# Performance work log

Measured on AMD Instinct MI355X. Metric: run time of the kernel, lower is better.

## Reference

```python
import jax, jax.numpy as jnp
import numpy as np

K = 3
STRIDE = 1
PADDING = 1
INVALID = -1.0


def _unfold(x, k, stride, padding, fill):
    # x: [B, C, H, W] -> patches [B, C, k, k, P] matching torch F.unfold ordering
    x = jnp.pad(x, ((0, 0), (0, 0), (padding, padding), (padding, padding)),
                constant_values=fill)
    # feature dim ordered channel-major (C, kh, kw), same as torch unfold
    p = jax.lax.conv_general_dilated_patches(x, (k, k), (stride, stride), 'VALID')
    b, _, ho, wo = p.shape
    c = x.shape[1]
    return p.reshape(b, c, k, k, ho * wo), ho, wo


def setup_inputs() -> dict:
    key = jax.random.key(0)
    k1, k2, k3, k4 = jax.random.split(key, 4)
    B, C, H, W = 8, 64, 128, 128
    OC = 64
    inp = jax.random.normal(k1, (B, C, H, W), dtype=jnp.float32)
    mask = jax.random.randint(k2, (B, H, W), 0, 4).astype(jnp.float32)
    conv = jax.random.normal(k3, (OC, C, K, K), dtype=jnp.float32) * 0.05
    bias = jax.random.normal(k4, (OC,), dtype=jnp.float32) * 0.05
    return {"inp": inp, "mask": mask, "conv": conv, "bias": bias}


def reference(inp, mask, conv, bias):
    k, stride, padding = K, STRIDE, PADDING
    b, c, h_in, w_in = inp.shape
    oc = conv.shape[0]
    center = (k - 1) // 2

    inp_patched, ho, wo = _unfold(inp, k, stride, padding, INVALID)       # [B,C,k,k,P]
    mask_patched, _, _ = _unfold(mask[:, None], k, stride, padding, INVALID)  # [B,1,k,k,P]
    mask_patched = mask_patched[:, 0]                                      # [B,k,k,P]

    center_val = mask_patched[:, center:center + 1, center:center + 1, :]  # [B,1,1,P]
    mask_eq = (mask_patched == center_val).astype(inp.dtype)               # [B,k,k,P]

    masked_input = inp_patched * mask_eq[:, None]                          # [B,C,k,k,P]
    m_norm = (k * k) / jnp.clip(mask_eq.reshape(b, k * k, -1).sum(axis=1), 1e-8)  # [B,P]

    masked_input = masked_input.reshape(b, c, k * k, -1)                   # [B,C,kk,P]
    w = conv.reshape(oc, c, k * k)                                         # [O,C,kk]
    out = jnp.einsum('bcxp,ocx->bop', masked_input, w)                     # [B,O,P]
    out = out * m_norm[:, None, :]
    out = out.reshape(b, oc, ho, wo)
    out = out + bias[None, :, None, None]

    mask_out = mask_patched[:, center, center, :].reshape(b, 1, ho, wo)
    return out, mask_out
```

## Files before the change

kernel.cpp:

```cpp
#include <hip/hip_runtime.h>
#include <stdint.h>

#define HW   128
#define CIN  64
#define OCN  64
#define NB   8

typedef __attribute__((ext_vector_type(8)))  short short8;
typedef __attribute__((ext_vector_type(16))) float floatx16;
typedef unsigned long long u64;

union F8 { short8 s; u64 u[2]; uint32_t d[4]; uint4 q; };

static __device__ __forceinline__ ushort f2bf(float f) {
    uint32_t u = __float_as_uint(f);
    uint32_t r = (u + 0x7FFFu + ((u >> 16) & 1u)) >> 16;
    return (ushort)r;
}

__global__ void wprep_kernel(const float* __restrict__ conv, ushort* __restrict__ wb) {
    int idx = blockIdx.x * 256 + threadIdx.x;
    int tap = idx >> 12;
    int r   = idx & 4095;
    int oc  = r >> 6;
    int c   = r & 63;
    wb[idx] = f2bf(conv[(oc * 64 + c) * 9 + tap]);
}

#define XS_CSTR 68
#define XS_ROW  (HW * XS_CSTR)
#define LDS_BYTES 72192

__global__ __launch_bounds__(256, 2)
void iconv_main(const float* __restrict__ inp, const float* __restrict__ mask,
                const ushort* __restrict__ wb, const float* __restrict__ bias,
                float* __restrict__ out)
{
    extern __shared__ char smem[];
    ushort* Xs = (ushort*)smem;
    float*  Ms = (float*)(smem + 69632);
    float*  Bb = (float*)(smem + 69632 + 2048);

    const int tid  = threadIdx.x;
    const int bb   = blockIdx.x >> 6;
    const int y0   = (blockIdx.x & 63) << 1;
    const int lane = tid & 63;
    const int l31  = lane & 31;
    const int lh   = lane >> 5;
    const int w    = tid >> 6;
    const int yloc = w >> 1;
    const int xw   = (w & 1) * 64;
    const int y    = y0 + yloc;

    {
        const int cp = tid & 31;
        const int xq = (tid >> 5) * 16;
        const float* base0 = inp + ((size_t)(bb * CIN + 2 * cp) * HW) * HW;
        #pragma unroll
        for (int rr = 0; rr < 4; ++rr) {
            int gy = y0 - 1 + rr;
            if (gy >= 0 && gy < HW) {
                const float4* q0 = (const float4*)(base0 + (size_t)gy * HW + xq);
                const float4* q1 = (const float4*)(base0 + (size_t)HW * HW + (size_t)gy * HW + xq);
                float4 v0[4], v1[4];
                #pragma unroll
                for (int i = 0; i < 4; ++i) { v0[i] = q0[i]; v1[i] = q1[i]; }
                ushort* xrow = Xs + rr * XS_ROW + xq * XS_CSTR + 2 * cp;
                const float* f0 = (const float*)v0;
                const float* f1 = (const float*)v1;
                #pragma unroll
                for (int i = 0; i < 16; ++i) {
                    uint32_t p = (uint32_t)f2bf(f0[i]) | ((uint32_t)f2bf(f1[i]) << 16);
                    *(uint32_t*)(xrow + i * XS_CSTR) = p;
                }
            }
        }
    }
    {
        int rr = tid >> 6, x0 = (tid & 63) * 2;
        int gy = y0 - 1 + rr;
        if (gy >= 0 && gy < HW) {
            float2 v = *(const float2*)(mask + ((size_t)bb * HW + gy) * HW + x0);
            Ms[rr * HW + x0]     = v.x;
            Ms[rr * HW + x0 + 1] = v.y;
        }
    }
    if (tid < OCN) Bb[tid] = bias[tid];

    {
        int r = tid >> 7, x = tid & 127;
        int gy = y0 + r;
        out[(size_t)NB * OCN * HW * HW + ((size_t)bb * HW + gy) * HW + x] =
            mask[((size_t)bb * HW + gy) * HW + x];
    }

    uint4 Areg[2][8];
    #pragma unroll
    for (int i = 0; i < 8; ++i) {
        int h = i >> 2, ks = i & 3;
        Areg[0][i] = *(const uint4*)(wb + (l31 + h * 32) * 64 + ks * 16 + lh * 8);
    }

    __syncthreads();

    uint32_t sel[9][2];
    float norm0, norm1;
    {
        int cnt0 = 0, cnt1 = 0;
        int xq0 = xw + l31, xq1 = xw + 32 + l31;
        float m00 = Ms[(1 + yloc) * HW + xq0];
        float m01 = Ms[(1 + yloc) * HW + xq1];
        #pragma unroll
        for (int t = 0; t < 9; ++t) {
            int dy = t / 3 - 1, dx = t % 3 - 1;
            int ny = y + dy;
            bool vy = (ny >= 0) && (ny < HW);
            int rbase = (1 + yloc + dy) * HW;
            {
                int nx = xq0 + dx;
                bool ok = vy && (nx >= 0) && (nx < HW);
                int nxc = nx < 0 ? 0 : (nx > HW - 1 ? HW - 1 : nx);
                bool eq = ok && (Ms[rbase + nxc] == m00);
                sel[t][0] = eq ? 0xFFFFFFFFu : 0u;
                cnt0 += eq ? 1 : 0;
            }
            {
                int nx = xq1 + dx;
                bool ok = vy && (nx >= 0) && (nx < HW);
                int nxc = nx < 0 ? 0 : (nx > HW - 1 ? HW - 1 : nx);
                bool eq = ok && (Ms[rbase + nxc] == m01);
                sel[t][1] = eq ? 0xFFFFFFFFu : 0u;
                cnt1 += eq ? 1 : 0;
            }
        }
        norm0 = 9.0f / (float)cnt0;
        norm1 = 9.0f / (float)cnt1;
    }

    floatx16 acc00 = {0,0,0,0,0,0,0,0,0,0,0,0,0,0,0,0};
    floatx16 acc01 = {0,0,0,0,0,0,0,0,0,0,0,0,0,0,0,0};
    floatx16 acc10 = {0,0,0,0,0,0,0,0,0,0,0,0,0,0,0,0};
    floatx16 acc11 = {0,0,0,0,0,0,0,0,0,0,0,0,0,0,0,0};

    #pragma unroll
    for (int t = 0; t < 9; ++t) {
        const int buf = t & 1, nbuf = buf ^ 1;
        if (t < 8) {
            const ushort* wp = wb + (t + 1) * 4096;
            #pragma unroll
            for (int i = 0; i < 8; ++i) {
                int h = i >> 2, ks = i & 3;
                Areg[nbuf][i] = *(const uint4*)(wp + (l31 + h * 32) * 64 + ks * 16 + lh * 8);
            }
        }

        const int dy = t / 3 - 1, dx = t % 3 - 1;
        const int rrB = 1 + yloc + dy;
        int xa = xw + l31 + dx;
        int xb0c = xa < 0 ? 0 : (xa > HW - 1 ? HW - 1 : xa);
        int xa1 = xa + 32;
        int xb1c = xa1 < 0 ? 0 : (xa1 > HW - 1 ? HW - 1 : xa1);
        const ushort* B0p = Xs + rrB * XS_ROW + xb0c * XS_CSTR + lh * 8;
        const ushort* B1p = Xs + rrB * XS_ROW + xb1c * XS_CSTR + lh * 8;
        const uint32_t s0 = sel[t][0], s1 = sel[t][1];

        #pragma unroll
        for (int ks = 0; ks < 4; ++ks) {
            F8 a0, a1, b0, b1;
            a0.q = Areg[buf][ks];
            a1.q = Areg[buf][4 + ks];
            b0.u[0] = *(const u64*)(B0p + ks * 16);
            b0.u[1] = *(const u64*)(B0p + ks * 16 + 4);
            b1.u[0] = *(const u64*)(B1p + ks * 16);
            b1.u[1] = *(const u64*)(B1p + ks * 16 + 4);
            b0.d[0] &= s0; b0.d[1] &= s0; b0.d[2] &= s0; b0.d[3] &= s0;
            b1.d[0] &= s1; b1.d[1] &= s1; b1.d[2] &= s1; b1.d[3] &= s1;
            acc00 = __builtin_amdgcn_mfma_f32_32x32x16_bf16(a0.s, b0.s, acc00, 0, 0, 0);
            acc01 = __builtin_amdgcn_mfma_f32_32x32x16_bf16(a0.s, b1.s, acc01, 0, 0, 0);
            acc10 = __builtin_amdgcn_mfma_f32_32x32x16_bf16(a1.s, b0.s, acc10, 0, 0, 0);
            acc11 = __builtin_amdgcn_mfma_f32_32x32x16_bf16(a1.s, b1.s, acc11, 0, 0, 0);
        }
    }

    float* outp = out + (size_t)bb * OCN * HW * HW + (size_t)y * HW;
    #pragma unroll
    for (int mt = 0; mt < 2; ++mt) {
        #pragma unroll
        for (int nt = 0; nt < 2; ++nt) {
            floatx16 a = (mt == 0) ? (nt == 0 ? acc00 : acc01)
                                   : (nt == 0 ? acc10 : acc11);
            float nm = (nt == 0) ? norm0 : norm1;
            int x = xw + nt * 32 + l31;
            #pragma unroll
            for (int r = 0; r < 16; ++r) {
                int oc = mt * 32 + (r & 3) + 8 * (r >> 2) + 4 * lh;
                outp[(size_t)oc * (HW * HW) + x] = a[r] * nm + Bb[oc];
            }
        }
    }
}

extern "C" void kernel_launch(void* const* d_in, const int* in_sizes, int n_in,
                              void* d_out, int out_size, void* d_ws, size_t ws_size,
                              hipStream_t stream) {
    (void)in_sizes; (void)n_in; (void)out_size; (void)ws_size;
    const float* inp  = (const float*)d_in[0];
    const float* mask = (const float*)d_in[1];
    const float* conv = (const float*)d_in[2];
    const float* bias = (const float*)d_in[3];
    float* out = (float*)d_out;
    ushort* wb = (ushort*)d_ws;

    hipFuncSetAttribute((const void*)iconv_main,
                        hipFuncAttributeMaxDynamicSharedMemorySize, LDS_BYTES);

    wprep_kernel<<<144, 256, 0, stream>>>(conv, wb);
    iconv_main<<<NB * (HW / 2), 256, LDS_BYTES, stream>>>(inp, mask, wb, bias, out);
}
```

Measured before the change: 110.5 us.

## Pre-transpose input to bf16 NHWC in prep kernel and load B tiles from global

```diff
diff --git a/kernel.cpp b/kernel.cpp
--- a/kernel.cpp
+++ b/kernel.cpp
@@ -8,171 +8,142 @@
 
 typedef __attribute__((ext_vector_type(8)))  short short8;
 typedef __attribute__((ext_vector_type(16))) float floatx16;
-typedef unsigned long long u64;
 
-union F8 { short8 s; u64 u[2]; uint32_t d[4]; uint4 q; };
+union F8 { short8 s; uint32_t d[4]; uint4 q; };
 
 static __device__ __forceinline__ ushort f2bf(float f) {
     uint32_t u = __float_as_uint(f);
-    uint32_t r = (u + 0x7FFFu + ((u >> 16) & 1u)) >> 16;
-    return (ushort)r;
+    return (ushort)((u + 0x7FFFu + ((u >> 16) & 1u)) >> 16);
 }
 
-__global__ void wprep_kernel(const float* __restrict__ conv, ushort* __restrict__ wb) {
-    int idx = blockIdx.x * 256 + threadIdx.x;
-    int tap = idx >> 12;
-    int r   = idx & 4095;
-    int oc  = r >> 6;
-    int c   = r & 63;
-    wb[idx] = f2bf(conv[(oc * 64 + c) * 9 + tap]);
+#define LROW_STR 68
+
+__global__ __launch_bounds__(256)
+void prep_kernel(const float* __restrict__ inp, const float* __restrict__ conv,
+                 ushort* __restrict__ wb, ushort* __restrict__ xb)
+{
+    __shared__ ushort Ls[HW * LROW_STR];
+    const int bid = blockIdx.x, tid = threadIdx.x;
+
+    if (bid >= 1024) {
+        int t = bid - 1024;
+        #pragma unroll
+        for (int i = 0; i < 16; ++i) {
+            int id = i * 256 + tid;
+            int oc = id >> 6, c = id & 63;
+            wb[t * 4096 + id] = f2bf(conv[(oc * 64 + c) * 9 + t]);
+        }
+        return;
+    }
+
+    const int bb = bid >> 7, y = bid & 127;
+    const int cg = tid >> 5, xg = tid & 31;
+    const float* src = inp + ((size_t)(bb * CIN + cg * 8) * HW + y) * HW + xg * 4;
+    #pragma unroll
+    for (int k = 0; k < 8; ++k) {
+        float4 v = *(const float4*)(src + (size_t)k * HW * HW);
+        ushort* p = Ls + (xg * 4) * LROW_STR + cg * 8 + k;
+        p[0]            = f2bf(v.x);
+        p[LROW_STR]     = f2bf(v.y);
+        p[2 * LROW_STR] = f2bf(v.z);
+        p[3 * LROW_STR] = f2bf(v.w);
+    }
+    __syncthreads();
+    ushort* dst = xb + (size_t)(bb * HW + y) * HW * 64;
+    const int g = tid & 7, p0 = tid >> 3;
+    #pragma unroll
+    for (int pass = 0; pass < 4; ++pass) {
+        int p = pass * 32 + p0;
+        uint2 a = *(const uint2*)(Ls + p * LROW_STR + g * 8);
+        uint2 b = *(const uint2*)(Ls + p * LROW_STR + g * 8 + 4);
+        *(uint4*)(dst + p * 64 + g * 8) = make_uint4(a.x, a.y, b.x, b.y);
+    }
 }
 
-#define XS_CSTR 68
-#define XS_ROW  (HW * XS_CSTR)
-#define LDS_BYTES 72192
+static __device__ __forceinline__ void load_tap(
+    const ushort* __restrict__ wb, const ushort* __restrict__ xb,
+    int t, int bb, int y, int x0, int x1, int l31, int lh,
+    uint4* Ar, uint4* Br)
+{
+    const ushort* wp = wb + t * 4096 + l31 * 64 + lh * 8;
+    #pragma unroll
+    for (int h = 0; h < 2; ++h)
+        #pragma unroll
+        for (int ks = 0; ks < 4; ++ks)
+            Ar[h * 4 + ks] = *(const uint4*)(wp + h * 2048 + ks * 16);
 
-__global__ __launch_bounds__(256, 2)
-void iconv_main(const float* __restrict__ inp, const float* __restrict__ mask,
-                const ushort* __restrict__ wb, const float* __restrict__ bias,
+    const int dy = t / 3 - 1, dx = t % 3 - 1;
+    int ny = y + dy; ny = ny < 0 ? 0 : (ny > HW - 1 ? HW - 1 : ny);
+    #pragma unroll
+    for (int n = 0; n < 2; ++n) {
+        int nx = (n ? x1 : x0) + dx;
+        nx = nx < 0 ? 0 : (nx > HW - 1 ? HW - 1 : nx);
+        const ushort* bp = xb + (((size_t)bb * HW + ny) * HW + nx) * 64 + lh * 8;
+        #pragma unroll
+        for (int ks = 0; ks < 4; ++ks)
+            Br[n * 4 + ks] = *(const uint4*)(bp + ks * 16);
+    }
+}
+
+__global__ __launch_bounds__(64, 2)
+void iconv_main(const ushort* __restrict__ xb, const ushort* __restrict__ wb,
+                const float* __restrict__ mask, const float* __restrict__ bias,
                 float* __restrict__ out)
 {
-    extern __shared__ char smem[];
-    ushort* Xs = (ushort*)smem;
-    float*  Ms = (float*)(smem + 69632);
-    float*  Bb = (float*)(smem + 69632 + 2048);
+    const int bid = blockIdx.x;
+    const int bb = bid >> 8, y = (bid >> 1) & 127, xw = (bid & 1) * 64;
+    const int lane = threadIdx.x, l31 = lane & 31, lh = lane >> 5;
+    const int x0 = xw + l31, x1 = x0 + 32;
 
-    const int tid  = threadIdx.x;
-    const int bb   = blockIdx.x >> 6;
-    const int y0   = (blockIdx.x & 63) << 1;
-    const int lane = tid & 63;
-    const int l31  = lane & 31;
-    const int lh   = lane >> 5;
-    const int w    = tid >> 6;
-    const int yloc = w >> 1;
-    const int xw   = (w & 1) * 64;
-    const int y    = y0 + yloc;
+    const float* mrow = mask + ((size_t)bb * HW + y) * HW;
+    const float m00 = mrow[x0], m01 = mrow[x1];
+    uint32_t bits0 = 0, bits1 = 0;
+    #pragma unroll
+    for (int t = 0; t < 9; ++t) {
+        int dy = t / 3 - 1, dx = t % 3 - 1;
+        int ny = y + dy;
+        bool vy = (ny >= 0) && (ny < HW);
+        int nyc = vy ? ny : y;
+        const float* r = mask + ((size_t)bb * HW + nyc) * HW;
+        int nx0 = x0 + dx, nx1 = x1 + dx;
+        bool ok0 = vy && (nx0 >= 0) && (nx0 < HW);
+        bool ok1 = vy && (nx1 >= 0) && (nx1 < HW);
+        int c0 = nx0 < 0 ? 0 : (nx0 > HW - 1 ? HW - 1 : nx0);
+        int c1 = nx1 < 0 ? 0 : (nx1 > HW - 1 ? HW - 1 : nx1);
+        if (ok0 && r[c0] == m00) bits0 |= 1u << t;
+        if (ok1 && r[c1] == m01) bits1 |= 1u << t;
+    }
+    const float norm0 = 9.0f / (float)__popc(bits0);
+    const float norm1 = 9.0f / (float)__popc(bits1);
 
-    {
-        const int cp = tid & 31;
-        const int xq = (tid >> 5) * 16;
-        const float* base0 = inp + ((size_t)(bb * CIN + 2 * cp) * HW) * HW;
-        #pragma unroll
-        for (int rr = 0; rr < 4; ++rr) {
-            int gy = y0 - 1 + rr;
-            if (gy >= 0 && gy < HW) {
-                const float4* q0 = (const float4*)(base0 + (size_t)gy * HW + xq);
-                const float4* q1 = (const float4*)(base0 + (size_t)HW * HW + (size_t)gy * HW + xq);
-                float4 v0[4], v1[4];
-                #pragma unroll
-                for (int i = 0; i < 4; ++i) { v0[i] = q0[i]; v1[i] = q1[i]; }
-                ushort* xrow = Xs + rr * XS_ROW + xq * XS_CSTR + 2 * cp;
-                const float* f0 = (const float*)v0;
-                const float* f1 = (const float*)v1;
-                #pragma unroll
-                for (int i = 0; i < 16; ++i) {
-                    uint32_t p = (uint32_t)f2bf(f0[i]) | ((uint32_t)f2bf(f1[i]) << 16);
-                    *(uint32_t*)(xrow + i * XS_CSTR) = p;
-                }
-            }
-        }
-    }
-    {
-        int rr = tid >> 6, x0 = (tid & 63) * 2;
-        int gy = y0 - 1 + rr;
-        if (gy >= 0 && gy < HW) {
-            float2 v = *(const float2*)(mask + ((size_t)bb * HW + gy) * HW + x0);
-            Ms[rr * HW + x0]     = v.x;
-            Ms[rr * HW + x0 + 1] = v.y;
-        }
-    }
-    if (tid < OCN) Bb[tid] = bias[tid];
-
-    {
-        int r = tid >> 7, x = tid & 127;
-        int gy = y0 + r;
-        out[(size_t)NB * OCN * HW * HW + ((size_t)bb * HW + gy) * HW + x] =
-            mask[((size_t)bb * HW + gy) * HW + x];
-    }
-
-    uint4 Areg[2][8];
-    #pragma unroll
-    for (int i = 0; i < 8; ++i) {
-        int h = i >> 2, ks = i & 3;
-        Areg[0][i] = *(const uint4*)(wb + (l31 + h * 32) * 64 + ks * 16 + lh * 8);
-    }
-
-    __syncthreads();
-
-    uint32_t sel[9][2];
-    float norm0, norm1;
-    {
-        int cnt0 = 0, cnt1 = 0;
-        int xq0 = xw + l31, xq1 = xw + 32 + l31;
-        float m00 = Ms[(1 + yloc) * HW + xq0];
-        float m01 = Ms[(1 + yloc) * HW + xq1];
-        #pragma unroll
-        for (int t = 0; t < 9; ++t) {
-            int dy = t / 3 - 1, dx = t % 3 - 1;
-            int ny = y + dy;
-            bool vy = (ny >= 0) && (ny < HW);
-            int rbase = (1 + yloc + dy) * HW;
-            {
-                int nx = xq0 + dx;
-                bool ok = vy && (nx >= 0) && (nx < HW);
-                int nxc = nx < 0 ? 0 : (nx > HW - 1 ? HW - 1 : nx);
-                bool eq = ok && (Ms[rbase + nxc] == m00);
-                sel[t][0] = eq ? 0xFFFFFFFFu : 0u;
-                cnt0 += eq ? 1 : 0;
-            }
-            {
-                int nx = xq1 + dx;
-                bool ok = vy && (nx >= 0) && (nx < HW);
-                int nxc = nx < 0 ? 0 : (nx > HW - 1 ? HW - 1 : nx);
-                bool eq = ok && (Ms[rbase + nxc] == m01);
-                sel[t][1] = eq ? 0xFFFFFFFFu : 0u;
-                cnt1 += eq ? 1 : 0;
-            }
-        }
-        norm0 = 9.0f / (float)cnt0;
-        norm1 = 9.0f / (float)cnt1;
-    }
+    float* mout = out + (size_t)NB * OCN * HW * HW + ((size_t)bb * HW + y) * HW;
+    mout[x0] = m00;
+    mout[x1] = m01;
 
     floatx16 acc00 = {0,0,0,0,0,0,0,0,0,0,0,0,0,0,0,0};
     floatx16 acc01 = {0,0,0,0,0,0,0,0,0,0,0,0,0,0,0,0};
     floatx16 acc10 = {0,0,0,0,0,0,0,0,0,0,0,0,0,0,0,0};
     floatx16 acc11 = {0,0,0,0,0,0,0,0,0,0,0,0,0,0,0,0};
 
+    uint4 Ar[2][8], Br[2][8];
+    load_tap(wb, xb, 0, bb, y, x0, x1, l31, lh, Ar[0], Br[0]);
+
     #pragma unroll
     for (int t = 0; t < 9; ++t) {
-        const int buf = t & 1, nbuf = buf ^ 1;
-        if (t < 8) {
-            const ushort* wp = wb + (t + 1) * 4096;
-            #pragma unroll
-            for (int i = 0; i < 8; ++i) {
-                int h = i >> 2, ks = i & 3;
-                Areg[nbuf][i] = *(const uint4*)(wp + (l31 + h * 32) * 64 + ks * 16 + lh * 8);
-            }
-        }
+        const int buf = t & 1;
+        if (t < 8)
+            load_tap(wb, xb, t + 1, bb, y, x0, x1, l31, lh, Ar[buf ^ 1], Br[buf ^ 1]);
 
-        const int dy = t / 3 - 1, dx = t % 3 - 1;
-        const int rrB = 1 + yloc + dy;
-        int xa = xw + l31 + dx;
-        int xb0c = xa < 0 ? 0 : (xa > HW - 1 ? HW - 1 : xa);
-        int xa1 = xa + 32;
-        int xb1c = xa1 < 0 ? 0 : (xa1 > HW - 1 ? HW - 1 : xa1);
-        const ushort* B0p = Xs + rrB * XS_ROW + xb0c * XS_CSTR + lh * 8;
-        const ushort* B1p = Xs + rrB * XS_ROW + xb1c * XS_CSTR + lh * 8;
-        const uint32_t s0 = sel[t][0], s1 = sel[t][1];
+        const uint32_t s0 = ((bits0 >> t) & 1u) ? 0xFFFFFFFFu : 0u;
+        const uint32_t s1 = ((bits1 >> t) & 1u) ? 0xFFFFFFFFu : 0u;
 
         #pragma unroll
         for (int ks = 0; ks < 4; ++ks) {
             F8 a0, a1, b0, b1;
-            a0.q = Areg[buf][ks];
-            a1.q = Areg[buf][4 + ks];
-            b0.u[0] = *(const u64*)(B0p + ks * 16);
-            b0.u[1] = *(const u64*)(B0p + ks * 16 + 4);
-            b1.u[0] = *(const u64*)(B1p + ks * 16);
-            b1.u[1] = *(const u64*)(B1p + ks * 16 + 4);
+            a0.q = Ar[buf][ks];
+            a1.q = Ar[buf][4 + ks];
+            b0.q = Br[buf][ks];
+            b1.q = Br[buf][4 + ks];
             b0.d[0] &= s0; b0.d[1] &= s0; b0.d[2] &= s0; b0.d[3] &= s0;
             b1.d[0] &= s1; b1.d[1] &= s1; b1.d[2] &= s1; b1.d[3] &= s1;
             acc00 = __builtin_amdgcn_mfma_f32_32x32x16_bf16(a0.s, b0.s, acc00, 0, 0, 0);
@@ -194,7 +165,7 @@
             #pragma unroll
             for (int r = 0; r < 16; ++r) {
                 int oc = mt * 32 + (r & 3) + 8 * (r >> 2) + 4 * lh;
-                outp[(size_t)oc * (HW * HW) + x] = a[r] * nm + Bb[oc];
+                outp[(size_t)oc * (HW * HW) + x] = a[r] * nm + bias[oc];
             }
         }
     }
@@ -209,11 +180,10 @@
     const float* conv = (const float*)d_in[2];
     const float* bias = (const float*)d_in[3];
     float* out = (float*)d_out;
+
     ushort* wb = (ushort*)d_ws;
+    ushort* xb = (ushort*)d_ws + 65536;
 
-    hipFuncSetAttribute((const void*)iconv_main,
-                        hipFuncAttributeMaxDynamicSharedMemorySize, LDS_BYTES);
-
-    wprep_kernel<<<144, 256, 0, stream>>>(conv, wb);
-    iconv_main<<<NB * (HW / 2), 256, LDS_BYTES, stream>>>(inp, mask, wb, bias, out);
+    prep_kernel<<<1033, 256, 0, stream>>>(inp, conv, wb, xb);
+    iconv_main<<<NB * HW * 2, 64, 0, stream>>>(xb, wb, mask, bias, out);
 }
```

Result: slower. 129.0 us (+16.7%).
